# Kernel optimization log

Measured on AMD Instinct MI355X. Metric: run time of the kernel, lower is better.

The kernel has to match this reference:

```python
import jax, jax.numpy as jnp
import numpy as np

D_MODEL = 256
D_FF = 1024
N_B = 4
LN_EPS = 1e-12


def setup_inputs() -> dict:
    key = jax.random.key(0)
    ks = jax.random.split(key, 8)
    B, T = 32, 2048
    x = jax.random.normal(ks[0], (B, T, D_MODEL), dtype=jnp.float32)
    b_seq = jax.random.randint(ks[1], (B, T), 0, N_B + 1, dtype=jnp.int32)
    # Per-behavior FFN params, stacked over branches (init std=0.02, zero bias)
    w1 = 0.02 * jax.random.normal(ks[2], (N_B, D_FF, D_MODEL), dtype=jnp.float32)
    b1 = jnp.zeros((N_B, D_FF), dtype=jnp.float32)
    w2 = 0.02 * jax.random.normal(ks[3], (N_B, D_MODEL, D_FF), dtype=jnp.float32)
    b2 = jnp.zeros((N_B, D_MODEL), dtype=jnp.float32)
    gamma = jnp.ones((N_B, D_MODEL), dtype=jnp.float32)
    beta = jnp.zeros((N_B, D_MODEL), dtype=jnp.float32)
    return {"x": x, "b_seq": b_seq, "w1": w1, "b1": b1, "w2": w2, "b2": b2, "gamma": gamma, "beta": beta}


def _layernorm(y, gamma, beta):
    # LN over last dim, eps=1e-12; gamma/beta broadcast over leading dims
    mu = jnp.mean(y, axis=-1, keepdims=True)
    var = jnp.mean((y - mu) ** 2, axis=-1, keepdims=True)
    return (y - mu) * jax.lax.rsqrt(var + LN_EPS) * gamma + beta


def reference(x, b_seq, w1, b1, w2, b2, gamma, beta):
    # x: [B,T,h]; run all n_b branch FFNs densely (faithful to original).
    h = jnp.einsum('bth,nfh->nbtf', x, w1) + b1[:, None, None, :]   # [n,B,T,f]
    h = jax.nn.elu(h)                                               # dropout is eval-mode identity
    y = jnp.einsum('nbtf,nhf->nbth', h, w2) + b2[:, None, None, :]  # [n,B,T,h]
    y = _layernorm(y, gamma[:, None, None, :], beta[:, None, None, :])
    # Prepend zeros branch (index 0), then one-hot select per token.
    stacked = jnp.concatenate([jnp.zeros_like(y[:1]), y], axis=0)   # [n+1,B,T,h]
    oh = jax.nn.one_hot(b_seq, N_B + 1, dtype=x.dtype)              # [B,T,n+1]
    return jnp.einsum('nbth,btn->bth', stacked, oh)
```

## Files before the change

kernel.cpp:

```cpp
#include <hip/hip_runtime.h>

#define TOK 65536
#define DM 256
#define DF 1024
#define NB 4

typedef unsigned short ushort_t;
typedef unsigned int uint32;

typedef __attribute__((ext_vector_type(8))) short bf16x8;
typedef __attribute__((ext_vector_type(4))) float f32x4;

__device__ inline ushort_t f2bf(float f) {
  union { float f; unsigned int u; } v; v.f = f;
  unsigned int u = v.u;
  unsigned int r = (u + 0x7FFFu + ((u >> 16) & 1u)) >> 16;
  return (ushort_t)r;
}
__device__ inline uint32 pack2(float a, float b) {
  return (uint32)f2bf(a) | ((uint32)f2bf(b) << 16);
}

__device__ __forceinline__ void dma16(const ushort_t* g, ushort_t* lds) {
  __builtin_amdgcn_global_load_lds(
      (const __attribute__((address_space(1))) unsigned int*)(const void*)g,
      (__attribute__((address_space(3))) unsigned int*)(void*)lds,
      16, 0, 0);
}

__global__ __launch_bounds__(256) void prep_weights_kernel(
    const float* __restrict__ w1, const float* __restrict__ w2,
    ushort_t* __restrict__ w1b, ushort_t* __restrict__ w2b,
    int* __restrict__ counts)
{
  if (blockIdx.x == 0 && blockIdx.y == 0 && threadIdx.x < NB)
    counts[threadIdx.x] = 0;
  const int idx = blockIdx.x * 256 + threadIdx.x;
  const float* src = blockIdx.y ? w2 : w1;
  ushort_t* dst = blockIdx.y ? w2b : w1b;
  f32x4 v = *(const f32x4*)(src + (size_t)idx * 4);
  uint2 p;
  p.x = pack2(v.x, v.y);
  p.y = pack2(v.z, v.w);
  *(uint2*)(dst + (size_t)idx * 4) = p;
}

__global__ __launch_bounds__(256) void route_kernel(
    const int* __restrict__ b_seq, int* __restrict__ counts,
    ushort_t* __restrict__ lists, uint32* __restrict__ out32)
{
  __shared__ int s_lpos[NB];
  __shared__ int s_lbase[NB];
  __shared__ int s_b[256];
  const int tid = threadIdx.x;
  const int base = blockIdx.x * 256;
  const int token = base + tid;
  if (tid < NB) s_lpos[tid] = 0;
  __syncthreads();
  const int b = b_seq[token];
  s_b[tid] = b;
  int my = 0;
  if (b > 0) my = atomicAdd(&s_lpos[b - 1], 1);
  __syncthreads();
  if (tid < NB) s_lbase[tid] = atomicAdd(&counts[tid], s_lpos[tid]);
  __syncthreads();
  if (b > 0) lists[(b - 1) * TOK + s_lbase[b - 1] + my] = (ushort_t)token;
  #pragma unroll 4
  for (int it = 0; it < 256; ++it) {
    int flat = it * 256 + tid;
    int tl = flat >> 8;
    int j = flat & 255;
    if (s_b[tl] == 0) out32[(size_t)(base + tl) * DM + j] = 0u;
  }
}

__global__ __launch_bounds__(256, 2) void ffn_kernel(
    const float* __restrict__ x,
    const ushort_t* __restrict__ w1b_all, const float* __restrict__ b1,
    const ushort_t* __restrict__ w2b_all, const float* __restrict__ b2,
    const float* __restrict__ gamma, const float* __restrict__ beta,
    const int* __restrict__ counts, const ushort_t* __restrict__ lists,
    float* __restrict__ out)
{
  const int id = blockIdx.x;
  const int slot = id & 7;
  const int n = slot >> 1;
  const int tile = ((id >> 3) << 1) + (slot & 1);
  const int cnt = counts[n];
  const int tile0 = tile * 64;
  if (tile0 >= cnt) return;
  const int mvalid = min(64, cnt - tile0);

  __shared__ __align__(16) ushort_t sWmem[32768];
  __shared__ __align__(16) ushort_t sH[64][40];
  __shared__ float sB1[DF];
  __shared__ int s_idx[64];
  __shared__ float s_ps[2][64];
  __shared__ float s_pq[2][64];
  __shared__ float s_mu[64];
  __shared__ float s_rs[64];

  ushort_t (*sX)[264] = (ushort_t (*)[264])sWmem;

  const int tid  = threadIdx.x;
  const int wv   = tid >> 6;
  const int lane = tid & 63;
  const int q    = lane >> 4;
  const int lc   = lane & 15;
  const int fi   = wv & 1;
  const int mh   = wv >> 1;
  const int dh   = wv & 1;

  const ushort_t* w1b = w1b_all + (size_t)n * DF * DM;
  const ushort_t* w2b = w2b_all + (size_t)n * DM * DF;

  if (tid < 64) {
    int i = tile0 + tid;
    s_idx[tid] = (int)lists[n * TOK + (i < cnt ? i : tile0)];
  }
  {
    f32x4 v = *(const f32x4*)(b1 + n * DF + tid * 4);
    *(f32x4*)(sB1 + tid * 4) = v;
  }
  __syncthreads();

  #pragma unroll
  for (int it = 0; it < 16; ++it) {
    int chunk = it * 256 + tid;
    int r = chunk >> 6;
    int c = (chunk & 63) << 2;
    f32x4 v = *(const f32x4*)(x + (size_t)s_idx[r] * DM + c);
    uint2 p;
    p.x = pack2(v.x, v.y);
    p.y = pack2(v.z, v.w);
    *(uint2*)(&sX[r][c]) = p;
  }
  __syncthreads();

  bf16x8 xfrag[2][8];
  #pragma unroll
  for (int mi2 = 0; mi2 < 2; ++mi2)
    #pragma unroll
    for (int ks = 0; ks < 8; ++ks)
      xfrag[mi2][ks] = *(const bf16x8*)(&sX[mh * 32 + mi2 * 16 + lc][ks * 32 + q * 8]);
  __syncthreads();

  auto issue_dma = [&](int fc1) {
    const int b = fc1 & 1;
    ushort_t* dW1 = sWmem + b * 8192;
    ushort_t* dW2 = sWmem + 16384 + b * 8192;
    const ushort_t* g1 = w1b + (size_t)(fc1 * 32) * DM;
    const ushort_t* g2 = w2b + fc1 * 32;
    #pragma unroll
    for (int j = 0; j < 4; ++j) {
      int i = wv * 4 + j;
      int s = i * 64 + lane;
      int r1 = s >> 5, cp1 = s & 31;
      dma16(g1 + (size_t)r1 * DM + (size_t)(cp1 ^ (r1 & 31)) * 8, dW1 + i * 512);
      int d2 = s >> 2, cp2 = s & 3;
      dma16(g2 + (size_t)d2 * DF + (size_t)(cp2 ^ (d2 & 3)) * 8, dW2 + i * 512);
    }
  };

  issue_dma(0);

  f32x4 yacc[2][8];
  #pragma unroll
  for (int mi2 = 0; mi2 < 2; ++mi2)
    #pragma unroll
    for (int di = 0; di < 8; ++di)
      yacc[mi2][di] = (f32x4){0.f, 0.f, 0.f, 0.f};

  #pragma unroll 1
  for (int fc = 0; fc < 32; ++fc) {
    const int b = fc & 1;
    const ushort_t* cW1 = sWmem + b * 8192;
    const ushort_t* cW2 = sWmem + 16384 + b * 8192;

    __builtin_amdgcn_sched_barrier(0);
    __builtin_amdgcn_s_waitcnt(0x0070);
    __builtin_amdgcn_s_barrier();
    __builtin_amdgcn_sched_barrier(0);

    if (fc < 31) issue_dma(fc + 1);

    f32x4 hacc[2];
    hacc[0] = (f32x4){0.f, 0.f, 0.f, 0.f};
    hacc[1] = (f32x4){0.f, 0.f, 0.f, 0.f};
    {
      const int r = fi * 16 + lc;
      #pragma unroll
      for (int ks = 0; ks < 8; ++ks) {
        int cp = (ks * 4 + q) ^ (r & 31);
        bf16x8 bf = *(const bf16x8*)(cW1 + r * 256 + cp * 8);
        hacc[0] = __builtin_amdgcn_mfma_f32_16x16x32_bf16(xfrag[0][ks], bf, hacc[0], 0, 0, 0);
        hacc[1] = __builtin_amdgcn_mfma_f32_16x16x32_bf16(xfrag[1][ks], bf, hacc[1], 0, 0, 0);
      }
    }
    const float b1v = sB1[fc * 32 + fi * 16 + lc];
    #pragma unroll
    for (int mi2 = 0; mi2 < 2; ++mi2) {
      #pragma unroll
      for (int r4 = 0; r4 < 4; ++r4) {
        float v = hacc[mi2][r4] + b1v;
        v = (v > 0.f) ? v : (__expf(v) - 1.f);
        sH[mh * 32 + mi2 * 16 + q * 4 + r4][fi * 16 + lc] = f2bf(v);
      }
    }

    __builtin_amdgcn_sched_barrier(0);
    __builtin_amdgcn_s_waitcnt(0xC07F);
    __builtin_amdgcn_s_barrier();
    __builtin_amdgcn_sched_barrier(0);

    bf16x8 af[2];
    #pragma unroll
    for (int mi2 = 0; mi2 < 2; ++mi2)
      af[mi2] = *(const bf16x8*)(&sH[mh * 32 + mi2 * 16 + lc][q * 8]);
    #pragma unroll
    for (int di = 0; di < 8; ++di) {
      int d = dh * 128 + di * 16 + lc;
      int cp = q ^ (d & 3);
      bf16x8 bf = *(const bf16x8*)(cW2 + d * 32 + cp * 8);
      yacc[0][di] = __builtin_amdgcn_mfma_f32_16x16x32_bf16(af[0], bf, yacc[0][di], 0, 0, 0);
      yacc[1][di] = __builtin_amdgcn_mfma_f32_16x16x32_bf16(af[1], bf, yacc[1][di], 0, 0, 0);
    }
  }

  __syncthreads();
  float b2v[8], gv[8], bv[8];
  #pragma unroll
  for (int di = 0; di < 8; ++di) {
    int dcol = n * DM + dh * 128 + di * 16 + lc;
    b2v[di] = b2[dcol];
    gv[di]  = gamma[dcol];
    bv[di]  = beta[dcol];
  }
  #pragma unroll
  for (int mi2 = 0; mi2 < 2; ++mi2)
    #pragma unroll
    for (int di = 0; di < 8; ++di)
      #pragma unroll
      for (int r4 = 0; r4 < 4; ++r4)
        yacc[mi2][di][r4] += b2v[di];

  #pragma unroll
  for (int mi2 = 0; mi2 < 2; ++mi2) {
    #pragma unroll
    for (int r4 = 0; r4 < 4; ++r4) {
      float s = 0.f, sq = 0.f;
      #pragma unroll
      for (int di = 0; di < 8; ++di) {
        float v = yacc[mi2][di][r4];
        s += v; sq += v * v;
      }
      #pragma unroll
      for (int off = 1; off < 16; off <<= 1) {
        s  += __shfl_xor(s, off, 64);
        sq += __shfl_xor(sq, off, 64);
      }
      if (lc == 0) {
        int tok = mh * 32 + mi2 * 16 + q * 4 + r4;
        s_ps[dh][tok] = s;
        s_pq[dh][tok] = sq;
      }
    }
  }
  __syncthreads();
  if (tid < 64) {
    float s  = s_ps[0][tid] + s_ps[1][tid];
    float sq = s_pq[0][tid] + s_pq[1][tid];
    float mu = s * (1.f / 256.f);
    float var = fmaxf(sq * (1.f / 256.f) - mu * mu, 0.f);
    s_mu[tid] = mu;
    s_rs[tid] = rsqrtf(var + 1e-12f);
  }
  __syncthreads();

  #pragma unroll
  for (int mi2 = 0; mi2 < 2; ++mi2) {
    #pragma unroll
    for (int r4 = 0; r4 < 4; ++r4) {
      int tok = mh * 32 + mi2 * 16 + q * 4 + r4;
      if (tok < mvalid) {
        float mu = s_mu[tok], rs = s_rs[tok];
        size_t rowbase = (size_t)s_idx[tok] * DM + dh * 128;
        #pragma unroll
        for (int di = 0; di < 8; ++di) {
          float v = (yacc[mi2][di][r4] - mu) * rs * gv[di] + bv[di];
          out[rowbase + di * 16 + lc] = v;
        }
      }
    }
  }
}

extern "C" void kernel_launch(void* const* d_in, const int* in_sizes, int n_in,
                              void* d_out, int out_size, void* d_ws, size_t ws_size,
                              hipStream_t stream) {
  const float* x     = (const float*)d_in[0];
  const int*   b_seq = (const int*)d_in[1];
  const float* w1    = (const float*)d_in[2];
  const float* b1    = (const float*)d_in[3];
  const float* w2    = (const float*)d_in[4];
  const float* b2    = (const float*)d_in[5];
  const float* gamma = (const float*)d_in[6];
  const float* beta  = (const float*)d_in[7];
  float* out = (float*)d_out;

  int* counts = (int*)d_ws;
  ushort_t* lists = (ushort_t*)((char*)d_ws + 256);
  ushort_t* w1b = (ushort_t*)((char*)d_ws + 256 + 512 * 1024);
  ushort_t* w2b = w1b + (size_t)NB * DF * DM;

  hipLaunchKernelGGL(prep_weights_kernel, dim3(1024, 2), dim3(256), 0, stream,
                     w1, w2, w1b, w2b, counts);
  hipLaunchKernelGGL(route_kernel, dim3(TOK / 256), dim3(256), 0, stream,
                     b_seq, counts, lists, (uint32*)d_out);
  hipLaunchKernelGGL(ffn_kernel, dim3(4096), dim3(256), 0, stream,
                     x, w1b, b1, w2b, b2, gamma, beta, counts, lists, out);
}
```

Before: 243.9 us.

## Grow FFN token tile to 96 with 6 waves and swizzled LDS layouts

Raises the per-block token tile from 64 to 96, using 384-thread blocks (6 waves, 3 blocks per CU), so each streamed weight chunk is reused across more tokens. It also XOR-swizzles the staged X tile and the W2 LDS layout to cut bank conflicts, stores b1 as bf16, adds s_setprio around MFMA loops, and widens the zero-fill stores in the routing kernel to 16 bytes. The larger tile raises register and LDS pressure, and a larger last tile per branch wastes more rows. Storing b1 in bf16 adds a small rounding change.

```diff
diff --git a/kernel.cpp b/kernel.cpp
--- a/kernel.cpp
+++ b/kernel.cpp
@@ -10,12 +10,16 @@
 
 typedef __attribute__((ext_vector_type(8))) short bf16x8;
 typedef __attribute__((ext_vector_type(4))) float f32x4;
+typedef __attribute__((ext_vector_type(4))) uint32 u32x4;
 
 __device__ inline ushort_t f2bf(float f) {
   union { float f; unsigned int u; } v; v.f = f;
   unsigned int u = v.u;
   unsigned int r = (u + 0x7FFFu + ((u >> 16) & 1u)) >> 16;
   return (ushort_t)r;
+}
+__device__ inline float bf2f(ushort_t u) {
+  union { unsigned int u; float f; } v; v.u = ((uint32)u) << 16; return v.f;
 }
 __device__ inline uint32 pack2(float a, float b) {
   return (uint32)f2bf(a) | ((uint32)f2bf(b) << 16);
@@ -47,7 +51,7 @@
 
 __global__ __launch_bounds__(256) void route_kernel(
     const int* __restrict__ b_seq, int* __restrict__ counts,
-    ushort_t* __restrict__ lists, uint32* __restrict__ out32)
+    ushort_t* __restrict__ lists, u32x4* __restrict__ out16)
 {
   __shared__ int s_lpos[NB];
   __shared__ int s_lbase[NB];
@@ -65,16 +69,17 @@
   if (tid < NB) s_lbase[tid] = atomicAdd(&counts[tid], s_lpos[tid]);
   __syncthreads();
   if (b > 0) lists[(b - 1) * TOK + s_lbase[b - 1] + my] = (ushort_t)token;
+  const u32x4 z = (u32x4){0u, 0u, 0u, 0u};
   #pragma unroll 4
-  for (int it = 0; it < 256; ++it) {
+  for (int it = 0; it < 64; ++it) {
     int flat = it * 256 + tid;
-    int tl = flat >> 8;
-    int j = flat & 255;
-    if (s_b[tl] == 0) out32[(size_t)(base + tl) * DM + j] = 0u;
-  }
-}
-
-__global__ __launch_bounds__(256, 2) void ffn_kernel(
+    int tl = flat >> 6;
+    int j = flat & 63;
+    if (s_b[tl] == 0) out16[(size_t)(base + tl) * 64 + j] = z;
+  }
+}
+
+__global__ __launch_bounds__(384, 3) void ffn_kernel(
     const float* __restrict__ x,
     const ushort_t* __restrict__ w1b_all, const float* __restrict__ b1,
     const ushort_t* __restrict__ w2b_all, const float* __restrict__ b2,
@@ -87,20 +92,20 @@
   const int n = slot >> 1;
   const int tile = ((id >> 3) << 1) + (slot & 1);
   const int cnt = counts[n];
-  const int tile0 = tile * 64;
+  const int tile0 = tile * 96;
   if (tile0 >= cnt) return;
-  const int mvalid = min(64, cnt - tile0);
+  const int mvalid = min(96, cnt - tile0);
 
   __shared__ __align__(16) ushort_t sWmem[32768];
-  __shared__ __align__(16) ushort_t sH[64][40];
-  __shared__ float sB1[DF];
-  __shared__ int s_idx[64];
-  __shared__ float s_ps[2][64];
-  __shared__ float s_pq[2][64];
-  __shared__ float s_mu[64];
-  __shared__ float s_rs[64];
-
-  ushort_t (*sX)[264] = (ushort_t (*)[264])sWmem;
+  __shared__ __align__(16) ushort_t sH[96][40];
+  __shared__ ushort_t sB1[DF];
+  __shared__ int s_idx[96];
+  __shared__ float s_ps[2][96];
+  __shared__ float s_pq[2][96];
+  __shared__ float s_mu[96];
+  __shared__ float s_rs[96];
+
+  ushort_t (*sX)[256] = (ushort_t (*)[256])sWmem;
 
   const int tid  = threadIdx.x;
   const int wv   = tid >> 6;
@@ -114,26 +119,31 @@
   const ushort_t* w1b = w1b_all + (size_t)n * DF * DM;
   const ushort_t* w2b = w2b_all + (size_t)n * DM * DF;
 
-  if (tid < 64) {
+  if (tid < 96) {
     int i = tile0 + tid;
     s_idx[tid] = (int)lists[n * TOK + (i < cnt ? i : tile0)];
   }
-  {
+  if (tid < 256) {
     f32x4 v = *(const f32x4*)(b1 + n * DF + tid * 4);
-    *(f32x4*)(sB1 + tid * 4) = v;
-  }
-  __syncthreads();
-
-  #pragma unroll
-  for (int it = 0; it < 16; ++it) {
-    int chunk = it * 256 + tid;
-    int r = chunk >> 6;
-    int c = (chunk & 63) << 2;
-    f32x4 v = *(const f32x4*)(x + (size_t)s_idx[r] * DM + c);
     uint2 p;
     p.x = pack2(v.x, v.y);
     p.y = pack2(v.z, v.w);
-    *(uint2*)(&sX[r][c]) = p;
+    *(uint2*)(sB1 + tid * 4) = p;
+  }
+  __syncthreads();
+
+  #pragma unroll
+  for (int it = 0; it < 8; ++it) {
+    int flat = it * 384 + tid;
+    int r = flat >> 5;
+    int c8 = flat & 31;
+    const float* xp = x + (size_t)s_idx[r] * DM + c8 * 8;
+    f32x4 a = *(const f32x4*)xp;
+    f32x4 c = *(const f32x4*)(xp + 4);
+    u32x4 p;
+    p.x = pack2(a.x, a.y); p.y = pack2(a.z, a.w);
+    p.z = pack2(c.x, c.y); p.w = pack2(c.z, c.w);
+    *(u32x4*)(&sX[r][(c8 ^ (r & 31)) * 8]) = p;
   }
   __syncthreads();
 
@@ -141,8 +151,11 @@
   #pragma unroll
   for (int mi2 = 0; mi2 < 2; ++mi2)
     #pragma unroll
-    for (int ks = 0; ks < 8; ++ks)
-      xfrag[mi2][ks] = *(const bf16x8*)(&sX[mh * 32 + mi2 * 16 + lc][ks * 32 + q * 8]);
+    for (int ks = 0; ks < 8; ++ks) {
+      int row = mh * 32 + mi2 * 16 + lc;
+      int g = (ks * 4 + q) ^ (row & 31);
+      xfrag[mi2][ks] = *(const bf16x8*)(&sX[row][g * 8]);
+    }
   __syncthreads();
 
   auto issue_dma = [&](int fc1) {
@@ -152,13 +165,16 @@
     const ushort_t* g1 = w1b + (size_t)(fc1 * 32) * DM;
     const ushort_t* g2 = w2b + fc1 * 32;
     #pragma unroll
-    for (int j = 0; j < 4; ++j) {
-      int i = wv * 4 + j;
-      int s = i * 64 + lane;
-      int r1 = s >> 5, cp1 = s & 31;
-      dma16(g1 + (size_t)r1 * DM + (size_t)(cp1 ^ (r1 & 31)) * 8, dW1 + i * 512);
-      int d2 = s >> 2, cp2 = s & 3;
-      dma16(g2 + (size_t)d2 * DF + (size_t)(cp2 ^ (d2 & 3)) * 8, dW2 + i * 512);
+    for (int j = 0; j < 3; ++j) {
+      int i = wv + j * 6;
+      if (i < 16) {
+        int s = i * 64 + lane;
+        int r1 = s >> 5, cp1 = s & 31;
+        dma16(g1 + (size_t)r1 * DM + (size_t)(cp1 ^ (r1 & 31)) * 8, dW1 + i * 512);
+        int d2 = s >> 2, cp2 = s & 3;
+        int cps = cp2 ^ (d2 & 3) ^ ((d2 >> 2) & 3);
+        dma16(g2 + (size_t)d2 * DF + (size_t)cps * 8, dW2 + i * 512);
+      }
     }
   };
 
@@ -184,28 +200,31 @@
 
     if (fc < 31) issue_dma(fc + 1);
 
-    f32x4 hacc[2];
-    hacc[0] = (f32x4){0.f, 0.f, 0.f, 0.f};
-    hacc[1] = (f32x4){0.f, 0.f, 0.f, 0.f};
+    const float b1v = bf2f(sB1[fc * 32 + fi * 16 + lc]);
+
+    f32x4 hacc0 = (f32x4){0.f, 0.f, 0.f, 0.f};
+    f32x4 hacc1 = (f32x4){0.f, 0.f, 0.f, 0.f};
     {
       const int r = fi * 16 + lc;
+      const ushort_t* w1row = cW1 + r * 256;
+      __builtin_amdgcn_s_setprio(1);
       #pragma unroll
       for (int ks = 0; ks < 8; ++ks) {
         int cp = (ks * 4 + q) ^ (r & 31);
-        bf16x8 bf = *(const bf16x8*)(cW1 + r * 256 + cp * 8);
-        hacc[0] = __builtin_amdgcn_mfma_f32_16x16x32_bf16(xfrag[0][ks], bf, hacc[0], 0, 0, 0);
-        hacc[1] = __builtin_amdgcn_mfma_f32_16x16x32_bf16(xfrag[1][ks], bf, hacc[1], 0, 0, 0);
-      }
-    }
-    const float b1v = sB1[fc * 32 + fi * 16 + lc];
-    #pragma unroll
-    for (int mi2 = 0; mi2 < 2; ++mi2) {
-      #pragma unroll
-      for (int r4 = 0; r4 < 4; ++r4) {
-        float v = hacc[mi2][r4] + b1v;
-        v = (v > 0.f) ? v : (__expf(v) - 1.f);
-        sH[mh * 32 + mi2 * 16 + q * 4 + r4][fi * 16 + lc] = f2bf(v);
-      }
+        bf16x8 bf = *(const bf16x8*)(w1row + cp * 8);
+        hacc0 = __builtin_amdgcn_mfma_f32_16x16x32_bf16(xfrag[0][ks], bf, hacc0, 0, 0, 0);
+        hacc1 = __builtin_amdgcn_mfma_f32_16x16x32_bf16(xfrag[1][ks], bf, hacc1, 0, 0, 0);
+      }
+      __builtin_amdgcn_s_setprio(0);
+    }
+    #pragma unroll
+    for (int r4 = 0; r4 < 4; ++r4) {
+      float v0 = hacc0[r4] + b1v;
+      v0 = (v0 > 0.f) ? v0 : (__expf(v0) - 1.f);
+      sH[mh * 32 + q * 4 + r4][fi * 16 + lc] = f2bf(v0);
+      float v1 = hacc1[r4] + b1v;
+      v1 = (v1 > 0.f) ? v1 : (__expf(v1) - 1.f);
+      sH[mh * 32 + 16 + q * 4 + r4][fi * 16 + lc] = f2bf(v1);
     }
 
     __builtin_amdgcn_sched_barrier(0);
@@ -217,13 +236,17 @@
     #pragma unroll
     for (int mi2 = 0; mi2 < 2; ++mi2)
       af[mi2] = *(const bf16x8*)(&sH[mh * 32 + mi2 * 16 + lc][q * 8]);
-    #pragma unroll
-    for (int di = 0; di < 8; ++di) {
-      int d = dh * 128 + di * 16 + lc;
-      int cp = q ^ (d & 3);
-      bf16x8 bf = *(const bf16x8*)(cW2 + d * 32 + cp * 8);
-      yacc[0][di] = __builtin_amdgcn_mfma_f32_16x16x32_bf16(af[0], bf, yacc[0][di], 0, 0, 0);
-      yacc[1][di] = __builtin_amdgcn_mfma_f32_16x16x32_bf16(af[1], bf, yacc[1][di], 0, 0, 0);
+    {
+      const int cpw = (q ^ (lc & 3) ^ (lc >> 2)) * 8;
+      const ushort_t* w2base = cW2 + (size_t)(dh * 128 + lc) * 32 + cpw;
+      __builtin_amdgcn_s_setprio(1);
+      #pragma unroll
+      for (int di = 0; di < 8; ++di) {
+        bf16x8 bf = *(const bf16x8*)(w2base + di * 512);
+        yacc[0][di] = __builtin_amdgcn_mfma_f32_16x16x32_bf16(af[0], bf, yacc[0][di], 0, 0, 0);
+        yacc[1][di] = __builtin_amdgcn_mfma_f32_16x16x32_bf16(af[1], bf, yacc[1][di], 0, 0, 0);
+      }
+      __builtin_amdgcn_s_setprio(0);
     }
   }
 
@@ -267,7 +290,7 @@
     }
   }
   __syncthreads();
-  if (tid < 64) {
+  if (tid < 96) {
     float s  = s_ps[0][tid] + s_ps[1][tid];
     float sq = s_pq[0][tid] + s_pq[1][tid];
     float mu = s * (1.f / 256.f);
@@ -316,7 +339,7 @@
   hipLaunchKernelGGL(prep_weights_kernel, dim3(1024, 2), dim3(256), 0, stream,
                      w1, w2, w1b, w2b, counts);
   hipLaunchKernelGGL(route_kernel, dim3(TOK / 256), dim3(256), 0, stream,
-                     b_seq, counts, lists, (uint32*)d_out);
-  hipLaunchKernelGGL(ffn_kernel, dim3(4096), dim3(256), 0, stream,
+                     b_seq, counts, lists, (u32x4*)d_out);
+  hipLaunchKernelGGL(ffn_kernel, dim3(2736), dim3(384), 0, stream,
                      x, w1b, b1, w2b, b2, gamma, beta, counts, lists, out);
 }
```

After: 404.3 us. 1.66x slower.
